# Optimization experiments

Measured on AMD Instinct MI355X. Metric: run time of the kernel, lower is better.

The kernel has to match this reference:

```python
import jax, jax.numpy as jnp
import numpy as np

N = 50000      # atoms
E = 800000     # edges (flat neighbor list)
ELEM = 64      # elem_fea_len
NBR = 64       # nbr_fea_len
EPS = 1e-5


def _bn(x, gamma, beta):
    # BatchNorm1d in training mode: biased batch stats over dim 0
    mean = jnp.mean(x, axis=0)
    var = jnp.mean(jnp.square(x - mean), axis=0)
    return (x - mean) * jax.lax.rsqrt(var + EPS) * gamma + beta


def setup_inputs() -> dict:
    key = jax.random.key(0)
    ks = jax.random.split(key, 8)
    atom_in_fea = jax.random.normal(ks[0], (N, ELEM), dtype=jnp.float32)
    nbr_fea = jax.random.normal(ks[1], (E, NBR), dtype=jnp.float32)
    self_fea_idx = jnp.sort(jax.random.randint(ks[2], (E,), 0, N))
    nbr_fea_idx = jax.random.randint(ks[3], (E,), 0, N)
    d_in = 2 * ELEM + NBR
    d_out = 2 * ELEM
    W = jax.random.normal(ks[4], (d_in, d_out), dtype=jnp.float32) / np.sqrt(d_in)
    b = jax.random.normal(ks[5], (d_out,), dtype=jnp.float32) * 0.01
    bn1_gamma = jnp.ones((d_out,), jnp.float32)
    bn1_beta = jnp.zeros((d_out,), jnp.float32)
    bn2_gamma = jnp.ones((ELEM,), jnp.float32)
    bn2_beta = jnp.zeros((ELEM,), jnp.float32)
    return {
        "atom_in_fea": atom_in_fea, "nbr_fea": nbr_fea,
        "self_fea_idx": self_fea_idx, "nbr_fea_idx": nbr_fea_idx,
        "W": W, "b": b,
        "bn1_gamma": bn1_gamma, "bn1_beta": bn1_beta,
        "bn2_gamma": bn2_gamma, "bn2_beta": bn2_beta,
    }


def reference(atom_in_fea, nbr_fea, self_fea_idx, nbr_fea_idx,
              W, b, bn1_gamma, bn1_beta, bn2_gamma, bn2_beta):
    n_atoms = atom_in_fea.shape[0]
    # gather endpoint features: (E, ELEM) each
    atom_self = atom_in_fea[self_fea_idx]
    atom_nbr = atom_in_fea[nbr_fea_idx]
    total = jnp.concatenate([atom_self, atom_nbr, nbr_fea], axis=1)  # (E, 2*ELEM+NBR)
    total = total @ W + b                                            # (E, 2*ELEM)
    total = _bn(total, bn1_gamma, bn1_beta)
    filter_fea, core_fea = jnp.split(total, 2, axis=1)
    nbr_msg = jax.nn.sigmoid(filter_fea) * jax.nn.softplus(core_fea)  # (E, ELEM)
    nbr_sumed = jax.ops.segment_sum(nbr_msg, self_fea_idx, num_segments=n_atoms)
    nbr_sumed = _bn(nbr_sumed, bn2_gamma, bn2_beta)
    return jax.nn.softplus(atom_in_fea + nbr_sumed)
```

## Files before the change

kernel.cpp:

```cpp
#include <hip/hip_runtime.h>

typedef unsigned short ushort_t;
typedef __attribute__((ext_vector_type(8))) short short8;
typedef __attribute__((ext_vector_type(4))) float f32x4;

constexpr int N_ATOMS = 50000;
constexpr int N_EDGES = 800000;
constexpr int ELEM    = 64;
constexpr int D_IN    = 192;
constexpr int D_OUT   = 128;
constexpr float EPS   = 1e-5f;

constexpr int TILE_M = 64;
constexpr int NREP   = 16;

constexpr size_t OFF_NS   = 0;
constexpr size_t OFF_ABF  = OFF_NS   + (size_t)N_ATOMS * ELEM * 4;
constexpr size_t OFF_WT   = OFF_ABF  + (size_t)N_ATOMS * ELEM * 2;
constexpr size_t OFF_BN1  = OFF_WT   + (size_t)D_OUT * D_IN * 2;
constexpr size_t OFF_SC1  = OFF_BN1  + NREP * 256 * 4;
constexpr size_t OFF_BN2  = OFF_SC1  + 256 * 4;
constexpr size_t OFF_SC2  = OFF_BN2  + NREP * 128 * 4;

__device__ __forceinline__ ushort_t f32_to_bf16(float f) {
    unsigned int u = __float_as_uint(f);
    u = (u + 0x7fffu + ((u >> 16) & 1u)) >> 16;
    return (ushort_t)u;
}
__device__ __forceinline__ float bf16_to_f32(ushort_t h) {
    return __uint_as_float(((unsigned int)h) << 16);
}
__device__ __forceinline__ float softplus_f(float x) {
    return fmaxf(x, 0.f) + __logf(1.f + __expf(-fabsf(x)));
}

__global__ void prep_init_kernel(const float* __restrict__ atom, const float* __restrict__ W,
                                 ushort_t* __restrict__ abf, ushort_t* __restrict__ Wt,
                                 float* __restrict__ ns,
                                 float* __restrict__ bn1r, float* __restrict__ bn2r) {
    int i = blockIdx.x * blockDim.x + threadIdx.x;
    if (i < N_ATOMS * ELEM) { abf[i] = f32_to_bf16(atom[i]); ns[i] = 0.f; }
    if (i < D_IN * D_OUT) {
        int k = i >> 7, n = i & 127;
        Wt[n * D_IN + k] = f32_to_bf16(W[i]);
    }
    if (i < NREP * 256) bn1r[i] = 0.f;
    if (i < NREP * 128) bn2r[i] = 0.f;
}

__device__ __forceinline__ void stage_A(ushort_t (*As)[200],
                                        const ushort_t* __restrict__ abf,
                                        const float* __restrict__ nbrf,
                                        const int* __restrict__ sidx,
                                        const int* __restrict__ nidx,
                                        int e0, int tid) {
    #pragma unroll
    for (int ch = 0; ch < 2; ++ch) {
        const int* __restrict__ idx = ch ? nidx : sidx;
        #pragma unroll
        for (int i = 0; i < 2; ++i) {
            int r = (tid >> 3) + 32 * i;
            int h = tid & 7;
            const uint4* src = (const uint4*)(abf + (size_t)idx[e0 + r] * 64);
            *(uint4*)&As[r][ch * 64 + h * 8] = src[h];
        }
    }
    #pragma unroll
    for (int i = 0; i < 4; ++i) {
        int r  = (tid >> 4) + 16 * i;
        int c4 = tid & 15;
        float4 v = *(const float4*)(nbrf + (size_t)(e0 + r) * 64 + c4 * 4);
        ushort4 pk;
        pk.x = f32_to_bf16(v.x); pk.y = f32_to_bf16(v.y);
        pk.z = f32_to_bf16(v.z); pk.w = f32_to_bf16(v.w);
        *(ushort4*)&As[r][128 + c4 * 4] = pk;
    }
}

__global__ __launch_bounds__(256) void stats_kernel(
    const ushort_t* __restrict__ abf, const float* __restrict__ nbrf,
    const int* __restrict__ sidx, const int* __restrict__ nidx,
    const ushort_t* __restrict__ Wt, const float* __restrict__ bias,
    float* __restrict__ bn1r)
{
    __shared__ __align__(16) ushort_t As[64][200];
    const int tid = threadIdx.x;
    const int e0  = blockIdx.x * TILE_M;

    stage_A(As, abf, nbrf, sidx, nidx, e0, tid);

    const int wave = tid >> 6, lane = tid & 63;
    const int m16 = lane & 15, quad = lane >> 4;

    short8 bfrag[2][6];
    #pragma unroll
    for (int nt = 0; nt < 2; ++nt) {
        const ushort_t* bp = Wt + (size_t)(wave * 32 + nt * 16 + m16) * D_IN + quad * 8;
        #pragma unroll
        for (int ks = 0; ks < 6; ++ks) bfrag[nt][ks] = *(const short8*)(bp + ks * 32);
    }
    __syncthreads();

    f32x4 acc[4][2];
    #pragma unroll
    for (int mt = 0; mt < 4; ++mt)
        #pragma unroll
        for (int nt = 0; nt < 2; ++nt) acc[mt][nt] = (f32x4){0.f, 0.f, 0.f, 0.f};

    #pragma unroll
    for (int ks = 0; ks < 6; ++ks) {
        int ko = ks * 32 + quad * 8;
        #pragma unroll
        for (int mt = 0; mt < 4; ++mt) {
            short8 a = *(const short8*)&As[mt * 16 + m16][ko];
            acc[mt][0] = __builtin_amdgcn_mfma_f32_16x16x32_bf16(a, bfrag[0][ks], acc[mt][0], 0, 0, 0);
            acc[mt][1] = __builtin_amdgcn_mfma_f32_16x16x32_bf16(a, bfrag[1][ks], acc[mt][1], 0, 0, 0);
        }
    }

    float* rep = bn1r + (size_t)(blockIdx.x & (NREP - 1)) * 256;
    #pragma unroll
    for (int nt = 0; nt < 2; ++nt) {
        int c = wave * 32 + nt * 16 + m16;
        float b = bias[c];
        float s = 0.f, q = 0.f;
        #pragma unroll
        for (int mt = 0; mt < 4; ++mt)
            #pragma unroll
            for (int r = 0; r < 4; ++r) {
                float v = acc[mt][nt][r] + b;
                s += v; q += v * v;
            }
        s += __shfl_xor(s, 16); s += __shfl_xor(s, 32);
        q += __shfl_xor(q, 16); q += __shfl_xor(q, 32);
        if (quad == 0) {
            atomicAdd(&rep[c], s);
            atomicAdd(&rep[128 + c], q);
        }
    }
}

__global__ void bn1_finalize(const float* __restrict__ bn1r,
                             const float* __restrict__ g1, const float* __restrict__ b1,
                             float* __restrict__ sc) {
    int c = threadIdx.x;
    float s = 0.f, q = 0.f;
    #pragma unroll
    for (int r = 0; r < NREP; ++r) { s += bn1r[r * 256 + c]; q += bn1r[r * 256 + 128 + c]; }
    float mean = s * (1.f / N_EDGES);
    float var  = q * (1.f / N_EDGES) - mean * mean;
    float scale = g1[c] * rsqrtf(var + EPS);
    sc[c] = scale;
    sc[128 + c] = b1[c] - mean * scale;
}

__global__ __launch_bounds__(256) void msg_kernel(
    const ushort_t* __restrict__ abf, const float* __restrict__ nbrf,
    const int* __restrict__ sidx, const int* __restrict__ nidx,
    const ushort_t* __restrict__ Wt, const float* __restrict__ bias,
    const float* __restrict__ sc, float* __restrict__ ns)
{
    __shared__ __align__(16) char smem[25600];
    ushort_t (*As)[200] = (ushort_t(*)[200])smem;
    float    (*Ms)[68]  = (float(*)[68])smem;
    __shared__ int ss[64];

    const int tid = threadIdx.x;
    const int e0  = blockIdx.x * TILE_M;

    stage_A(As, abf, nbrf, sidx, nidx, e0, tid);
    if (tid < 64) ss[tid] = sidx[e0 + tid];

    const int wave = tid >> 6, lane = tid & 63;
    const int m16 = lane & 15, quad = lane >> 4;
    const int cf = wave * 16 + m16;
    const int cc = 64 + cf;

    short8 bfrag[2][6];
    {
        const ushort_t* bp0 = Wt + (size_t)cf * D_IN + quad * 8;
        const ushort_t* bp1 = Wt + (size_t)cc * D_IN + quad * 8;
        #pragma unroll
        for (int ks = 0; ks < 6; ++ks) {
            bfrag[0][ks] = *(const short8*)(bp0 + ks * 32);
            bfrag[1][ks] = *(const short8*)(bp1 + ks * 32);
        }
    }
    __syncthreads();

    f32x4 acc[4][2];
    #pragma unroll
    for (int mt = 0; mt < 4; ++mt)
        #pragma unroll
        for (int nt = 0; nt < 2; ++nt) acc[mt][nt] = (f32x4){0.f, 0.f, 0.f, 0.f};

    #pragma unroll
    for (int ks = 0; ks < 6; ++ks) {
        int ko = ks * 32 + quad * 8;
        #pragma unroll
        for (int mt = 0; mt < 4; ++mt) {
            short8 a = *(const short8*)&As[mt * 16 + m16][ko];
            acc[mt][0] = __builtin_amdgcn_mfma_f32_16x16x32_bf16(a, bfrag[0][ks], acc[mt][0], 0, 0, 0);
            acc[mt][1] = __builtin_amdgcn_mfma_f32_16x16x32_bf16(a, bfrag[1][ks], acc[mt][1], 0, 0, 0);
        }
    }
    __syncthreads();

    {
        float bf_ = bias[cf], bc_ = bias[cc];
        float scf = sc[cf], shf = sc[128 + cf];
        float scc = sc[cc], shc = sc[128 + cc];
        #pragma unroll
        for (int mt = 0; mt < 4; ++mt) {
            int row = mt * 16 + quad * 4;
            #pragma unroll
            for (int r = 0; r < 4; ++r) {
                float yf = fmaf(acc[mt][0][r] + bf_, scf, shf);
                float yc = fmaf(acc[mt][1][r] + bc_, scc, shc);
                Ms[row + r][cf] = softplus_f(yc) / (1.f + __expf(-yf));
            }
        }
    }
    __syncthreads();

    {
        int v = tid >> 6, c = tid & 63;
        int base = v * 16;
        int cur = ss[base];
        float a = 0.f;
        #pragma unroll
        for (int r = 0; r < 16; ++r) {
            int s = ss[base + r];
            if (s != cur) { atomicAdd(&ns[(size_t)cur * 64 + c], a); cur = s; a = 0.f; }
            a += Ms[base + r][c];
        }
        atomicAdd(&ns[(size_t)cur * 64 + c], a);
    }
}

__global__ __launch_bounds__(256) void bn2_stats_kernel(
    const float* __restrict__ ns, float* __restrict__ bn2r)
{
    int c = threadIdx.x & 63;
    float s = 0.f, q = 0.f;
    for (int a = blockIdx.x * 4 + (threadIdx.x >> 6); a < N_ATOMS; a += 4096) {
        float v = ns[a * ELEM + c];
        s += v; q += v * v;
    }
    float* rep = bn2r + (size_t)(blockIdx.x & (NREP - 1)) * 128;
    atomicAdd(&rep[c], s);
    atomicAdd(&rep[64 + c], q);
}

__global__ void bn2_finalize(const float* __restrict__ bn2r,
                             const float* __restrict__ g2, const float* __restrict__ b2,
                             float* __restrict__ sc2) {
    int c = threadIdx.x;
    float s = 0.f, q = 0.f;
    #pragma unroll
    for (int r = 0; r < NREP; ++r) { s += bn2r[r * 128 + c]; q += bn2r[r * 128 + 64 + c]; }
    float mean = s * (1.f / N_ATOMS);
    float var  = q * (1.f / N_ATOMS) - mean * mean;
    float scale = g2[c] * rsqrtf(var + EPS);
    sc2[c] = scale;
    sc2[64 + c] = b2[c] - mean * scale;
}

__global__ void final_kernel(const float* __restrict__ atom, const float* __restrict__ ns,
                             const float* __restrict__ sc2, float* __restrict__ out)
{
    int i = blockIdx.x * blockDim.x + threadIdx.x;
    if (i < N_ATOMS * ELEM) {
        int c = i & 63;
        float x = atom[i] + fmaf(ns[i], sc2[c], sc2[64 + c]);
        out[i] = softplus_f(x);
    }
}

extern "C" void kernel_launch(void* const* d_in, const int* in_sizes, int n_in,
                              void* d_out, int out_size, void* d_ws, size_t ws_size,
                              hipStream_t stream) {
    const float* atom = (const float*)d_in[0];
    const float* nbrf = (const float*)d_in[1];
    const int*   sidx = (const int*)d_in[2];
    const int*   nidx = (const int*)d_in[3];
    const float* W    = (const float*)d_in[4];
    const float* bias = (const float*)d_in[5];
    const float* g1   = (const float*)d_in[6];
    const float* b1   = (const float*)d_in[7];
    const float* g2   = (const float*)d_in[8];
    const float* b2   = (const float*)d_in[9];
    float* out = (float*)d_out;
    char*  ws  = (char*)d_ws;

    float*    ns   = (float*)(ws + OFF_NS);
    ushort_t* abf  = (ushort_t*)(ws + OFF_ABF);
    ushort_t* Wt   = (ushort_t*)(ws + OFF_WT);
    float*    bn1r = (float*)(ws + OFF_BN1);
    float*    sc1  = (float*)(ws + OFF_SC1);
    float*    bn2r = (float*)(ws + OFF_BN2);
    float*    sc2  = (float*)(ws + OFF_SC2);

    hipLaunchKernelGGL(prep_init_kernel, dim3((N_ATOMS * ELEM + 255) / 256), dim3(256), 0, stream,
                       atom, W, abf, Wt, ns, bn1r, bn2r);
    hipLaunchKernelGGL(stats_kernel, dim3(N_EDGES / TILE_M), dim3(256), 0, stream,
                       abf, nbrf, sidx, nidx, Wt, bias, bn1r);
    hipLaunchKernelGGL(bn1_finalize, dim3(1), dim3(128), 0, stream, bn1r, g1, b1, sc1);
    hipLaunchKernelGGL(msg_kernel, dim3(N_EDGES / TILE_M), dim3(256), 0, stream,
                       abf, nbrf, sidx, nidx, Wt, bias, sc1, ns);
    hipLaunchKernelGGL(bn2_stats_kernel, dim3(1024), dim3(256), 0, stream, ns, bn2r);
    hipLaunchKernelGGL(bn2_finalize, dim3(1), dim3(64), 0, stream, bn2r, g2, b2, sc2);
    hipLaunchKernelGGL(final_kernel, dim3((N_ATOMS * ELEM + 255) / 256), dim3(256), 0, stream,
                       atom, ns, sc2, out);
}
```

Before: 460.0 us.

## Load GEMM operands straight into MFMA registers and reduce segments with shuffles

Both GEMM kernels stop staging gathered edge rows in LDS. Each lane now loads its edge's bf16 atom features and converts nbr_fea straight into MFMA B fragments, with W as the A operand, and every block loops over a fixed chunk of 16-edge groups while prefetching the next indices. The message kernel replaces the LDS transpose and serial per-column segment sum with a 16-lane segmented shuffle scan followed by atomics. The linear bias is dropped because training-mode BatchNorm cancels it. This removes LDS traffic and barriers, but all four waves of a block now gather the same edge rows, leaning on the caches.

```diff
diff --git a/kernel.cpp b/kernel.cpp
--- a/kernel.cpp
+++ b/kernel.cpp
@@ -11,8 +11,12 @@
 constexpr int D_OUT   = 128;
 constexpr float EPS   = 1e-5f;
 
-constexpr int TILE_M = 64;
 constexpr int NREP   = 16;
+
+constexpr int NGROUPS     = N_EDGES / 16;
+constexpr int GEMM_BLOCKS = 5000;
+constexpr int CHUNK       = NGROUPS / GEMM_BLOCKS;
+static_assert(NGROUPS % GEMM_BLOCKS == 0, "even split");
 
 constexpr size_t OFF_NS   = 0;
 constexpr size_t OFF_ABF  = OFF_NS   + (size_t)N_ATOMS * ELEM * 4;
@@ -27,11 +31,16 @@
     u = (u + 0x7fffu + ((u >> 16) & 1u)) >> 16;
     return (ushort_t)u;
 }
-__device__ __forceinline__ float bf16_to_f32(ushort_t h) {
-    return __uint_as_float(((unsigned int)h) << 16);
-}
 __device__ __forceinline__ float softplus_f(float x) {
     return fmaxf(x, 0.f) + __logf(1.f + __expf(-fabsf(x)));
+}
+__device__ __forceinline__ short8 pack8(float4 a, float4 b) {
+    short8 r;
+    r[0] = (short)f32_to_bf16(a.x); r[1] = (short)f32_to_bf16(a.y);
+    r[2] = (short)f32_to_bf16(a.z); r[3] = (short)f32_to_bf16(a.w);
+    r[4] = (short)f32_to_bf16(b.x); r[5] = (short)f32_to_bf16(b.y);
+    r[6] = (short)f32_to_bf16(b.z); r[7] = (short)f32_to_bf16(b.w);
+    return r;
 }
 
 __global__ void prep_init_kernel(const float* __restrict__ atom, const float* __restrict__ W,
@@ -48,96 +57,86 @@
     if (i < NREP * 128) bn2r[i] = 0.f;
 }
 
-__device__ __forceinline__ void stage_A(ushort_t (*As)[200],
-                                        const ushort_t* __restrict__ abf,
-                                        const float* __restrict__ nbrf,
-                                        const int* __restrict__ sidx,
-                                        const int* __restrict__ nidx,
-                                        int e0, int tid) {
-    #pragma unroll
-    for (int ch = 0; ch < 2; ++ch) {
-        const int* __restrict__ idx = ch ? nidx : sidx;
-        #pragma unroll
-        for (int i = 0; i < 2; ++i) {
-            int r = (tid >> 3) + 32 * i;
-            int h = tid & 7;
-            const uint4* src = (const uint4*)(abf + (size_t)idx[e0 + r] * 64);
-            *(uint4*)&As[r][ch * 64 + h * 8] = src[h];
-        }
-    }
-    #pragma unroll
-    for (int i = 0; i < 4; ++i) {
-        int r  = (tid >> 4) + 16 * i;
-        int c4 = tid & 15;
-        float4 v = *(const float4*)(nbrf + (size_t)(e0 + r) * 64 + c4 * 4);
-        ushort4 pk;
-        pk.x = f32_to_bf16(v.x); pk.y = f32_to_bf16(v.y);
-        pk.z = f32_to_bf16(v.z); pk.w = f32_to_bf16(v.w);
-        *(ushort4*)&As[r][128 + c4 * 4] = pk;
-    }
+__device__ __forceinline__ void load_bfrags(short8 (&bf)[6],
+                                            const ushort_t* __restrict__ abf,
+                                            const float* __restrict__ nbrf,
+                                            int si, int ni, int e, int quad) {
+    bf[0] = *(const short8*)(abf + (size_t)si * 64 +      quad * 8);
+    bf[1] = *(const short8*)(abf + (size_t)si * 64 + 32 + quad * 8);
+    bf[2] = *(const short8*)(abf + (size_t)ni * 64 +      quad * 8);
+    bf[3] = *(const short8*)(abf + (size_t)ni * 64 + 32 + quad * 8);
+    const float* pf = nbrf + (size_t)e * 64 + quad * 8;
+    float4 a0 = *(const float4*)(pf);
+    float4 a1 = *(const float4*)(pf + 4);
+    float4 b0 = *(const float4*)(pf + 32);
+    float4 b1 = *(const float4*)(pf + 36);
+    bf[4] = pack8(a0, a1);
+    bf[5] = pack8(b0, b1);
 }
 
 __global__ __launch_bounds__(256) void stats_kernel(
     const ushort_t* __restrict__ abf, const float* __restrict__ nbrf,
     const int* __restrict__ sidx, const int* __restrict__ nidx,
-    const ushort_t* __restrict__ Wt, const float* __restrict__ bias,
-    float* __restrict__ bn1r)
+    const ushort_t* __restrict__ Wt, float* __restrict__ bn1r)
 {
-    __shared__ __align__(16) ushort_t As[64][200];
-    const int tid = threadIdx.x;
-    const int e0  = blockIdx.x * TILE_M;
-
-    stage_A(As, abf, nbrf, sidx, nidx, e0, tid);
-
+    const int tid  = threadIdx.x;
     const int wave = tid >> 6, lane = tid & 63;
-    const int m16 = lane & 15, quad = lane >> 4;
-
-    short8 bfrag[2][6];
-    #pragma unroll
-    for (int nt = 0; nt < 2; ++nt) {
-        const ushort_t* bp = Wt + (size_t)(wave * 32 + nt * 16 + m16) * D_IN + quad * 8;
-        #pragma unroll
-        for (int ks = 0; ks < 6; ++ks) bfrag[nt][ks] = *(const short8*)(bp + ks * 32);
-    }
-    __syncthreads();
-
-    f32x4 acc[4][2];
-    #pragma unroll
-    for (int mt = 0; mt < 4; ++mt)
-        #pragma unroll
-        for (int nt = 0; nt < 2; ++nt) acc[mt][nt] = (f32x4){0.f, 0.f, 0.f, 0.f};
-
-    #pragma unroll
-    for (int ks = 0; ks < 6; ++ks) {
-        int ko = ks * 32 + quad * 8;
-        #pragma unroll
-        for (int mt = 0; mt < 4; ++mt) {
-            short8 a = *(const short8*)&As[mt * 16 + m16][ko];
-            acc[mt][0] = __builtin_amdgcn_mfma_f32_16x16x32_bf16(a, bfrag[0][ks], acc[mt][0], 0, 0, 0);
-            acc[mt][1] = __builtin_amdgcn_mfma_f32_16x16x32_bf16(a, bfrag[1][ks], acc[mt][1], 0, 0, 0);
-        }
-    }
-
-    float* rep = bn1r + (size_t)(blockIdx.x & (NREP - 1)) * 256;
-    #pragma unroll
-    for (int nt = 0; nt < 2; ++nt) {
-        int c = wave * 32 + nt * 16 + m16;
-        float b = bias[c];
-        float s = 0.f, q = 0.f;
-        #pragma unroll
-        for (int mt = 0; mt < 4; ++mt)
+    const int m16  = lane & 15, quad = lane >> 4;
+    const int wid  = blockIdx.x;
+
+    short8 wfrag[2][6];
+    #pragma unroll
+    for (int t = 0; t < 2; ++t) {
+        const ushort_t* wp = Wt + (size_t)(t * 64 + wave * 16 + m16) * D_IN + quad * 8;
+        #pragma unroll
+        for (int ks = 0; ks < 6; ++ks) wfrag[t][ks] = *(const short8*)(wp + ks * 32);
+    }
+
+    float s[2][4] = {{0.f,0.f,0.f,0.f},{0.f,0.f,0.f,0.f}};
+    float q[2][4] = {{0.f,0.f,0.f,0.f},{0.f,0.f,0.f,0.f}};
+
+    const int g0 = wid * CHUNK;
+    int e  = g0 * 16 + m16;
+    int si = sidx[e], ni = nidx[e];
+    for (int g = g0; g < g0 + CHUNK; ++g) {
+        int e_n  = e + ((g + 1 < g0 + CHUNK) ? 16 : 0);
+        int si_n = sidx[e_n], ni_n = nidx[e_n];
+
+        short8 bf[6];
+        load_bfrags(bf, abf, nbrf, si, ni, e, quad);
+
+        f32x4 acc0 = {0.f,0.f,0.f,0.f}, acc1 = {0.f,0.f,0.f,0.f};
+        #pragma unroll
+        for (int ks = 0; ks < 6; ++ks) {
+            acc0 = __builtin_amdgcn_mfma_f32_16x16x32_bf16(wfrag[0][ks], bf[ks], acc0, 0, 0, 0);
+            acc1 = __builtin_amdgcn_mfma_f32_16x16x32_bf16(wfrag[1][ks], bf[ks], acc1, 0, 0, 0);
+        }
+        #pragma unroll
+        for (int r = 0; r < 4; ++r) {
+            float v0 = acc0[r], v1 = acc1[r];
+            s[0][r] += v0; q[0][r] += v0 * v0;
+            s[1][r] += v1; q[1][r] += v1 * v1;
+        }
+        e = e_n; si = si_n; ni = ni_n;
+    }
+
+    float* rep = bn1r + (size_t)(wid & (NREP - 1)) * 256;
+    #pragma unroll
+    for (int t = 0; t < 2; ++t)
+        #pragma unroll
+        for (int r = 0; r < 4; ++r) {
+            float sv = s[t][r], qv = q[t][r];
             #pragma unroll
-            for (int r = 0; r < 4; ++r) {
-                float v = acc[mt][nt][r] + b;
-                s += v; q += v * v;
+            for (int d = 1; d < 16; d <<= 1) {
+                sv += __shfl_xor(sv, d);
+                qv += __shfl_xor(qv, d);
             }
-        s += __shfl_xor(s, 16); s += __shfl_xor(s, 32);
-        q += __shfl_xor(q, 16); q += __shfl_xor(q, 32);
-        if (quad == 0) {
-            atomicAdd(&rep[c], s);
-            atomicAdd(&rep[128 + c], q);
-        }
-    }
+            if (m16 == 0) {
+                int c = t * 64 + wave * 16 + quad * 4 + r;
+                atomicAdd(&rep[c], sv);
+                atomicAdd(&rep[128 + c], qv);
+            }
+        }
 }
 
 __global__ void bn1_finalize(const float* __restrict__ bn1r,
@@ -157,84 +156,74 @@
 __global__ __launch_bounds__(256) void msg_kernel(
     const ushort_t* __restrict__ abf, const float* __restrict__ nbrf,
     const int* __restrict__ sidx, const int* __restrict__ nidx,
-    const ushort_t* __restrict__ Wt, const float* __restrict__ bias,
-    const float* __restrict__ sc, float* __restrict__ ns)
+    const ushort_t* __restrict__ Wt, const float* __restrict__ sc,
+    float* __restrict__ ns)
 {
-    __shared__ __align__(16) char smem[25600];
-    ushort_t (*As)[200] = (ushort_t(*)[200])smem;
-    float    (*Ms)[68]  = (float(*)[68])smem;
-    __shared__ int ss[64];
-
-    const int tid = threadIdx.x;
-    const int e0  = blockIdx.x * TILE_M;
-
-    stage_A(As, abf, nbrf, sidx, nidx, e0, tid);
-    if (tid < 64) ss[tid] = sidx[e0 + tid];
-
+    const int tid  = threadIdx.x;
     const int wave = tid >> 6, lane = tid & 63;
-    const int m16 = lane & 15, quad = lane >> 4;
-    const int cf = wave * 16 + m16;
-    const int cc = 64 + cf;
-
-    short8 bfrag[2][6];
-    {
-        const ushort_t* bp0 = Wt + (size_t)cf * D_IN + quad * 8;
-        const ushort_t* bp1 = Wt + (size_t)cc * D_IN + quad * 8;
+    const int m16  = lane & 15, quad = lane >> 4;
+    const int wid  = blockIdx.x;
+
+    short8 wfrag[2][6];
+    #pragma unroll
+    for (int t = 0; t < 2; ++t) {
+        const ushort_t* wp = Wt + (size_t)(t * 64 + wave * 16 + m16) * D_IN + quad * 8;
+        #pragma unroll
+        for (int ks = 0; ks < 6; ++ks) wfrag[t][ks] = *(const short8*)(wp + ks * 32);
+    }
+
+    float scf[4], shf[4], scc[4], shc[4];
+    #pragma unroll
+    for (int r = 0; r < 4; ++r) {
+        int cf = wave * 16 + quad * 4 + r;
+        scf[r] = sc[cf];       shf[r] = sc[128 + cf];
+        scc[r] = sc[64 + cf];  shc[r] = sc[192 + cf];
+    }
+
+    const int g0 = wid * CHUNK;
+    int e  = g0 * 16 + m16;
+    int si = sidx[e], ni = nidx[e];
+    for (int g = g0; g < g0 + CHUNK; ++g) {
+        int e_n  = e + ((g + 1 < g0 + CHUNK) ? 16 : 0);
+        int si_n = sidx[e_n], ni_n = nidx[e_n];
+        const int a_self = si;
+
+        short8 bf[6];
+        load_bfrags(bf, abf, nbrf, si, ni, e, quad);
+
+        f32x4 acc0 = {0.f,0.f,0.f,0.f}, acc1 = {0.f,0.f,0.f,0.f};
         #pragma unroll
         for (int ks = 0; ks < 6; ++ks) {
-            bfrag[0][ks] = *(const short8*)(bp0 + ks * 32);
-            bfrag[1][ks] = *(const short8*)(bp1 + ks * 32);
-        }
-    }
-    __syncthreads();
-
-    f32x4 acc[4][2];
-    #pragma unroll
-    for (int mt = 0; mt < 4; ++mt)
-        #pragma unroll
-        for (int nt = 0; nt < 2; ++nt) acc[mt][nt] = (f32x4){0.f, 0.f, 0.f, 0.f};
-
-    #pragma unroll
-    for (int ks = 0; ks < 6; ++ks) {
-        int ko = ks * 32 + quad * 8;
-        #pragma unroll
-        for (int mt = 0; mt < 4; ++mt) {
-            short8 a = *(const short8*)&As[mt * 16 + m16][ko];
-            acc[mt][0] = __builtin_amdgcn_mfma_f32_16x16x32_bf16(a, bfrag[0][ks], acc[mt][0], 0, 0, 0);
-            acc[mt][1] = __builtin_amdgcn_mfma_f32_16x16x32_bf16(a, bfrag[1][ks], acc[mt][1], 0, 0, 0);
-        }
-    }
-    __syncthreads();
-
-    {
-        float bf_ = bias[cf], bc_ = bias[cc];
-        float scf = sc[cf], shf = sc[128 + cf];
-        float scc = sc[cc], shc = sc[128 + cc];
-        #pragma unroll
-        for (int mt = 0; mt < 4; ++mt) {
-            int row = mt * 16 + quad * 4;
-            #pragma unroll
-            for (int r = 0; r < 4; ++r) {
-                float yf = fmaf(acc[mt][0][r] + bf_, scf, shf);
-                float yc = fmaf(acc[mt][1][r] + bc_, scc, shc);
-                Ms[row + r][cf] = softplus_f(yc) / (1.f + __expf(-yf));
-            }
-        }
-    }
-    __syncthreads();
-
-    {
-        int v = tid >> 6, c = tid & 63;
-        int base = v * 16;
-        int cur = ss[base];
-        float a = 0.f;
-        #pragma unroll
-        for (int r = 0; r < 16; ++r) {
-            int s = ss[base + r];
-            if (s != cur) { atomicAdd(&ns[(size_t)cur * 64 + c], a); cur = s; a = 0.f; }
-            a += Ms[base + r][c];
-        }
-        atomicAdd(&ns[(size_t)cur * 64 + c], a);
+            acc0 = __builtin_amdgcn_mfma_f32_16x16x32_bf16(wfrag[0][ks], bf[ks], acc0, 0, 0, 0);
+            acc1 = __builtin_amdgcn_mfma_f32_16x16x32_bf16(wfrag[1][ks], bf[ks], acc1, 0, 0, 0);
+        }
+
+        float m[4];
+        #pragma unroll
+        for (int r = 0; r < 4; ++r) {
+            float yf = fmaf(acc0[r], scf[r], shf[r]);
+            float yc = fmaf(acc1[r], scc[r], shc[r]);
+            m[r] = softplus_f(yc) / (1.f + __expf(-yf));
+        }
+
+        int a = a_self;
+        #pragma unroll
+        for (int d = 1; d < 16; d <<= 1) {
+            int   au = __shfl_up(a,    d, 16);
+            float u0 = __shfl_up(m[0], d, 16);
+            float u1 = __shfl_up(m[1], d, 16);
+            float u2 = __shfl_up(m[2], d, 16);
+            float u3 = __shfl_up(m[3], d, 16);
+            if (m16 >= d && au == a) { m[0] += u0; m[1] += u1; m[2] += u2; m[3] += u3; }
+        }
+        int an = __shfl_down(a, 1, 16);
+        if (m16 == 15 || an != a) {
+            float* p = ns + (size_t)a * 64 + wave * 16 + quad * 4;
+            atomicAdd(p + 0, m[0]); atomicAdd(p + 1, m[1]);
+            atomicAdd(p + 2, m[2]); atomicAdd(p + 3, m[3]);
+        }
+
+        e = e_n; si = si_n; ni = ni_n;
     }
 }
 
@@ -285,7 +274,6 @@
     const int*   sidx = (const int*)d_in[2];
     const int*   nidx = (const int*)d_in[3];
     const float* W    = (const float*)d_in[4];
-    const float* bias = (const float*)d_in[5];
     const float* g1   = (const float*)d_in[6];
     const float* b1   = (const float*)d_in[7];
     const float* g2   = (const float*)d_in[8];
@@ -303,11 +291,11 @@
 
     hipLaunchKernelGGL(prep_init_kernel, dim3((N_ATOMS * ELEM + 255) / 256), dim3(256), 0, stream,
                        atom, W, abf, Wt, ns, bn1r, bn2r);
-    hipLaunchKernelGGL(stats_kernel, dim3(N_EDGES / TILE_M), dim3(256), 0, stream,
-                       abf, nbrf, sidx, nidx, Wt, bias, bn1r);
+    hipLaunchKernelGGL(stats_kernel, dim3(GEMM_BLOCKS), dim3(256), 0, stream,
+                       abf, nbrf, sidx, nidx, Wt, bn1r);
     hipLaunchKernelGGL(bn1_finalize, dim3(1), dim3(128), 0, stream, bn1r, g1, b1, sc1);
-    hipLaunchKernelGGL(msg_kernel, dim3(N_EDGES / TILE_M), dim3(256), 0, stream,
-                       abf, nbrf, sidx, nidx, Wt, bias, sc1, ns);
+    hipLaunchKernelGGL(msg_kernel, dim3(GEMM_BLOCKS), dim3(256), 0, stream,
+                       abf, nbrf, sidx, nidx, Wt, sc1, ns);
     hipLaunchKernelGGL(bn2_stats_kernel, dim3(1024), dim3(256), 0, stream, ns, bn2r);
     hipLaunchKernelGGL(bn2_finalize, dim3(1), dim3(64), 0, stream, bn2r, g2, b2, sc2);
     hipLaunchKernelGGL(final_kernel, dim3((N_ATOMS * ELEM + 255) / 256), dim3(256), 0, stream,
```

After: 677.1 us. +47.2%, slower.
